# Kernel tuning notes

Hardware: AMD Instinct MI355X
Metric: run time of the kernel (lower is better)

## Reference

```python
import jax, jax.numpy as jnp
import numpy as np

N_ELEC = 62      # electrodes per graph (fixed by RGNN/SEED)
BATCH = 4096     # number of graphs
IN_CH = 5
HID = 32
N_CLS = 3
K = 2            # SGConv propagation steps (num_layers)


def setup_inputs() -> dict:
    key = jax.random.key(0)
    k1, k2, k3, k4 = jax.random.split(key, 4)
    n_tril = N_ELEC * (N_ELEC + 1) // 2  # 1953 learned lower-tri weights
    x = jax.random.normal(k1, (BATCH * N_ELEC, IN_CH), jnp.float32)
    adj_tril = jax.random.uniform(k2, (n_tril,), jnp.float32)
    lin_w = jax.random.normal(k3, (HID, IN_CH), jnp.float32) * 0.3
    lin_b = jnp.zeros((HID,), jnp.float32)
    fc_w = jax.random.normal(k4, (N_CLS, HID), jnp.float32) * 0.2
    fc_b = jnp.zeros((N_CLS,), jnp.float32)
    # Dense per-graph edge list matching adj.reshape(-1).repeat(B):
    # edge e = b*3844 + i*62 + j has source row=b*62+i, target col=b*62+j.
    i = np.arange(N_ELEC, dtype=np.int32)
    src = np.repeat(i, N_ELEC)              # [3844]
    dst = np.tile(i, N_ELEC)                # [3844]
    off = (np.arange(BATCH, dtype=np.int32) * N_ELEC)[:, None]
    row = (src[None, :] + off).reshape(-1)  # [B*3844]
    col = (dst[None, :] + off).reshape(-1)
    edge_index = jnp.asarray(np.stack([row, col]))  # int32 [2, E]
    batch_idx = jnp.asarray(np.repeat(np.arange(BATCH, dtype=np.int32), N_ELEC))
    return dict(x=x, adj_tril=adj_tril, lin_w=lin_w, lin_b=lin_b,
                fc_w=fc_w, fc_b=fc_b, edge_index=edge_index, batch_idx=batch_idx)


def reference(x, adj_tril, lin_w, lin_b, fc_w, fc_b, edge_index, batch_idx):
    # Rebuild symmetric dense adjacency from learned lower-triangular params.
    xs, ys = np.tril_indices(N_ELEC)  # static indices
    A = jnp.zeros((N_ELEC, N_ELEC), x.dtype).at[xs, ys].set(adj_tril)
    A = A + A.T - jnp.diag(jnp.diag(A))
    w = jnp.tile(A.reshape(-1), BATCH)        # edge weights [E]
    row, col = edge_index[0], edge_index[1]
    n_nodes = BATCH * N_ELEC
    # Symmetric GCN norm: D^-1/2 A D^-1/2 over the edge list (self-loops
    # already present in the dense graph, so add_remaining_self_loops is a
    # pure edge reorder here).
    deg = jax.ops.segment_sum(jnp.abs(w), row, num_segments=n_nodes)
    safe_deg = jnp.where(deg > 0, deg, 1.0)
    dinv = jnp.where(deg > 0, jax.lax.rsqrt(safe_deg), 0.0)
    norm = dinv[row] * w * dinv[col]          # [E]
    # K rounds of gather-scale-scatter propagation (SGConv).
    h = x
    for _ in range(K):
        h = jax.ops.segment_sum(norm[:, None] * h[row], col, num_segments=n_nodes)
    h = jax.nn.relu(h @ lin_w.T + lin_b)       # SGConv linear + relu
    pooled = jax.ops.segment_sum(h, batch_idx, num_segments=BATCH)  # global_add_pool
    # dropout is identity in eval mode
    return pooled @ fc_w.T + fc_b              # [B, num_classes]
```

## Files before the change

kernel.cpp:

```cpp
#include <hip/hip_runtime.h>

#define NE 62
#define IC 5
#define HID 32
#define NCLS 3
#define NGRAPH 4096
#define NTRIL 1953
#define SA 68
#define NM (NE*SA)

__global__ __launch_bounds__(256) void build_M(const float* __restrict__ adj_tril,
                                               float* __restrict__ Mg) {
    __shared__ float A[NE * SA];
    __shared__ float dinv[NE];
    int tid = threadIdx.x;
    for (int t = tid; t < NTRIL; t += 256) {
        float v = adj_tril[t];
        float r = sqrtf((float)(8 * t + 1));
        int i = (int)((r - 1.0f) * 0.5f);
        while ((i + 1) * (i + 2) / 2 <= t) ++i;
        while (i * (i + 1) / 2 > t) --i;
        int j = t - i * (i + 1) / 2;
        A[i * SA + j] = v;
        A[j * SA + i] = v;
    }
    __syncthreads();
    if (tid < NE) {
        float s = 0.f;
        for (int k = 0; k < NE; ++k) s += fabsf(A[tid * SA + k]);
        dinv[tid] = (s > 0.f) ? rsqrtf(s) : 0.f;
    }
    __syncthreads();
    for (int g = tid; g < NE * NE; g += 256) {
        int i = g / NE, j = g % NE;
        A[i * SA + j] *= dinv[i] * dinv[j];
    }
    __syncthreads();
    int g = blockIdx.x * 256 + tid;
    if (g < NE * NE) {
        int i = g / NE, j = g % NE;
        const float4* ra = (const float4*)(A + i * SA);
        const float4* rb = (const float4*)(A + j * SA);
        float acc = 0.f;
#pragma unroll
        for (int c = 0; c < 15; ++c) {
            float4 a = ra[c], b = rb[c];
            acc += a.x * b.x + a.y * b.y + a.z * b.z + a.w * b.w;
        }
        acc += A[i * SA + 60] * A[j * SA + 60] + A[i * SA + 61] * A[j * SA + 61];
        Mg[i * SA + j] = acc;
    }
}

__global__ __launch_bounds__(256) void forward_k(const float* __restrict__ x,
        const float* __restrict__ lin_w, const float* __restrict__ lin_b,
        const float* __restrict__ fc_w, const float* __restrict__ fc_b,
        const float* __restrict__ Mg, float* __restrict__ out) {
    __shared__ float Mlds[NM];
    __shared__ float Ys[4][NE * 12];
    int tid = threadIdx.x;
    {
        const float4* src = (const float4*)Mg;
        float4* dst = (float4*)Mlds;
        for (int t = tid; t < NM / 4; t += 256) dst[t] = src[t];
    }
    int wid = tid >> 6;
    int lane = tid & 63;
    int b = blockIdx.x * 4 + wid;
    int bu = __builtin_amdgcn_readfirstlane(b);
    const float* xg = x + (size_t)bu * (NE * IC);
    int c = lane & 31;
    float w0 = lin_w[c * 5 + 0], w1 = lin_w[c * 5 + 1], w2 = lin_w[c * 5 + 2],
          w3 = lin_w[c * 5 + 3], w4 = lin_w[c * 5 + 4];
    float lb = lin_b[c];
    float f0 = fc_w[c], f1 = fc_w[32 + c], f2 = fc_w[64 + c];
    __syncthreads();
    int j = lane;
    if (j < NE) {
        float y0 = 0, y1 = 0, y2 = 0, y3 = 0, y4 = 0;
        const float4* Mrow = (const float4*)(Mlds + j * SA);
        for (int ch = 0; ch < 15; ++ch) {
            float4 m = Mrow[ch];
            const float* xi = xg + ch * 20;
            y0 += m.x * xi[0];  y1 += m.x * xi[1];  y2 += m.x * xi[2];  y3 += m.x * xi[3];  y4 += m.x * xi[4];
            y0 += m.y * xi[5];  y1 += m.y * xi[6];  y2 += m.y * xi[7];  y3 += m.y * xi[8];  y4 += m.y * xi[9];
            y0 += m.z * xi[10]; y1 += m.z * xi[11]; y2 += m.z * xi[12]; y3 += m.z * xi[13]; y4 += m.z * xi[14];
            y0 += m.w * xi[15]; y1 += m.w * xi[16]; y2 += m.w * xi[17]; y3 += m.w * xi[18]; y4 += m.w * xi[19];
        }
        float m60 = Mlds[j * SA + 60], m61 = Mlds[j * SA + 61];
        y0 += m60 * xg[300] + m61 * xg[305];
        y1 += m60 * xg[301] + m61 * xg[306];
        y2 += m60 * xg[302] + m61 * xg[307];
        y3 += m60 * xg[303] + m61 * xg[308];
        y4 += m60 * xg[304] + m61 * xg[309];
        float* yr = &Ys[wid][j * 12];
        *(float4*)yr = make_float4(y0, y1, y2, y3);
        yr[4] = y4;
    }
    __syncthreads();
    int half = lane >> 5;
    float acc = 0.f;
    int jbeg = half * 31;
    for (int t = 0; t < 31; ++t) {
        const float* yr = &Ys[wid][(jbeg + t) * 12];
        float4 yv = *(const float4*)yr;
        float d = yv.x * w0 + yv.y * w1 + yv.z * w2 + yv.w * w3 + yr[4] * w4 + lb;
        acc += fmaxf(d, 0.f);
    }
    acc += __shfl_xor(acc, 32, 64);
    float p0 = acc * f0, p1 = acc * f1, p2 = acc * f2;
#pragma unroll
    for (int m = 16; m >= 1; m >>= 1) {
        p0 += __shfl_xor(p0, m, 64);
        p1 += __shfl_xor(p1, m, 64);
        p2 += __shfl_xor(p2, m, 64);
    }
    if (lane == 0) {
        out[b * 3 + 0] = p0 + fc_b[0];
        out[b * 3 + 1] = p1 + fc_b[1];
        out[b * 3 + 2] = p2 + fc_b[2];
    }
}

extern "C" void kernel_launch(void* const* d_in, const int* in_sizes, int n_in,
                              void* d_out, int out_size, void* d_ws, size_t ws_size,
                              hipStream_t stream) {
    const float* x        = (const float*)d_in[0];
    const float* adj_tril = (const float*)d_in[1];
    const float* lin_w    = (const float*)d_in[2];
    const float* lin_b    = (const float*)d_in[3];
    const float* fc_w     = (const float*)d_in[4];
    const float* fc_b     = (const float*)d_in[5];
    float* out = (float*)d_out;
    float* Mg  = (float*)d_ws;

    build_M<<<16, 256, 0, stream>>>(adj_tril, Mg);
    forward_k<<<1024, 256, 0, stream>>>(x, lin_w, lin_b, fc_w, fc_b, Mg, out);
}
```

Measured before the change: 185.1 us.

## Reorder M into column-chunk layout and stage x tiles in LDS

M is now written in a chunk-major layout (groups of 4 columns across all rows, plus a tail block), so lanes read consecutive float4s from LDS without conflicts. Each block cooperatively loads the x data for its 4 graphs into shared memory with coalesced float2 loads, and the inner loop reads x from LDS as float4. Before, each lane read x through uniform scalar global loads. The change adds LDS usage and an extra staging phase, which may affect occupancy.

```diff
diff --git a/kernel.cpp b/kernel.cpp
--- a/kernel.cpp
+++ b/kernel.cpp
@@ -2,12 +2,9 @@
 
 #define NE 62
 #define IC 5
-#define HID 32
-#define NCLS 3
-#define NGRAPH 4096
 #define NTRIL 1953
 #define SA 68
-#define NM (NE*SA)
+#define MTOT 3844
 
 __global__ __launch_bounds__(256) void build_M(const float* __restrict__ adj_tril,
                                                float* __restrict__ Mg) {
@@ -38,17 +35,19 @@
     __syncthreads();
     int g = blockIdx.x * 256 + tid;
     if (g < NE * NE) {
-        int i = g / NE, j = g % NE;
-        const float4* ra = (const float4*)(A + i * SA);
-        const float4* rb = (const float4*)(A + j * SA);
+        int r = g / NE, cidx = g % NE;
+        const float4* ra = (const float4*)(A + r * SA);
+        const float4* rb = (const float4*)(A + cidx * SA);
         float acc = 0.f;
 #pragma unroll
         for (int c = 0; c < 15; ++c) {
             float4 a = ra[c], b = rb[c];
             acc += a.x * b.x + a.y * b.y + a.z * b.z + a.w * b.w;
         }
-        acc += A[i * SA + 60] * A[j * SA + 60] + A[i * SA + 61] * A[j * SA + 61];
-        Mg[i * SA + j] = acc;
+        acc += A[r * SA + 60] * A[cidx * SA + 60] + A[r * SA + 61] * A[cidx * SA + 61];
+        int addr = (cidx < 60) ? ((cidx >> 2) * 248 + r * 4 + (cidx & 3))
+                               : (3720 + r * 2 + (cidx - 60));
+        Mg[addr] = acc;
     }
 }
 
@@ -56,19 +55,23 @@
         const float* __restrict__ lin_w, const float* __restrict__ lin_b,
         const float* __restrict__ fc_w, const float* __restrict__ fc_b,
         const float* __restrict__ Mg, float* __restrict__ out) {
-    __shared__ float Mlds[NM];
+    __shared__ float Mlds[MTOT];
+    __shared__ float Xs[4 * 312];
     __shared__ float Ys[4][NE * 12];
     int tid = threadIdx.x;
     {
         const float4* src = (const float4*)Mg;
         float4* dst = (float4*)Mlds;
-        for (int t = tid; t < NM / 4; t += 256) dst[t] = src[t];
+        for (int t = tid; t < MTOT / 4; t += 256) dst[t] = src[t];
+        const float2* xsrc = (const float2*)(x + (size_t)blockIdx.x * (4 * 310));
+        for (int t = tid; t < 620; t += 256) {
+            int w = t / 155, o = t - w * 155;
+            *(float2*)&Xs[w * 312 + o * 2] = xsrc[t];
+        }
     }
     int wid = tid >> 6;
     int lane = tid & 63;
     int b = blockIdx.x * 4 + wid;
-    int bu = __builtin_amdgcn_readfirstlane(b);
-    const float* xg = x + (size_t)bu * (NE * IC);
     int c = lane & 31;
     float w0 = lin_w[c * 5 + 0], w1 = lin_w[c * 5 + 1], w2 = lin_w[c * 5 + 2],
           w3 = lin_w[c * 5 + 3], w4 = lin_w[c * 5 + 4];
@@ -77,22 +80,25 @@
     __syncthreads();
     int j = lane;
     if (j < NE) {
+        const float* xb = Xs + wid * 312;
         float y0 = 0, y1 = 0, y2 = 0, y3 = 0, y4 = 0;
-        const float4* Mrow = (const float4*)(Mlds + j * SA);
+#pragma unroll
         for (int ch = 0; ch < 15; ++ch) {
-            float4 m = Mrow[ch];
-            const float* xi = xg + ch * 20;
-            y0 += m.x * xi[0];  y1 += m.x * xi[1];  y2 += m.x * xi[2];  y3 += m.x * xi[3];  y4 += m.x * xi[4];
-            y0 += m.y * xi[5];  y1 += m.y * xi[6];  y2 += m.y * xi[7];  y3 += m.y * xi[8];  y4 += m.y * xi[9];
-            y0 += m.z * xi[10]; y1 += m.z * xi[11]; y2 += m.z * xi[12]; y3 += m.z * xi[13]; y4 += m.z * xi[14];
-            y0 += m.w * xi[15]; y1 += m.w * xi[16]; y2 += m.w * xi[17]; y3 += m.w * xi[18]; y4 += m.w * xi[19];
+            float4 m = *(const float4*)(Mlds + ch * 248 + j * 4);
+            const float4* xi = (const float4*)(xb + ch * 20);
+            float4 xa = xi[0], xv = xi[1], xc = xi[2], xd = xi[3], xe = xi[4];
+            y0 += m.x * xa.x; y1 += m.x * xa.y; y2 += m.x * xa.z; y3 += m.x * xa.w; y4 += m.x * xv.x;
+            y0 += m.y * xv.y; y1 += m.y * xv.z; y2 += m.y * xv.w; y3 += m.y * xc.x; y4 += m.y * xc.y;
+            y0 += m.z * xc.z; y1 += m.z * xc.w; y2 += m.z * xd.x; y3 += m.z * xd.y; y4 += m.z * xd.z;
+            y0 += m.w * xd.w; y1 += m.w * xe.x; y2 += m.w * xe.y; y3 += m.w * xe.z; y4 += m.w * xe.w;
         }
-        float m60 = Mlds[j * SA + 60], m61 = Mlds[j * SA + 61];
-        y0 += m60 * xg[300] + m61 * xg[305];
-        y1 += m60 * xg[301] + m61 * xg[306];
-        y2 += m60 * xg[302] + m61 * xg[307];
-        y3 += m60 * xg[303] + m61 * xg[308];
-        y4 += m60 * xg[304] + m61 * xg[309];
+        float2 mt = *(const float2*)(Mlds + 3720 + j * 2);
+        const float* xt = xb + 300;
+        y0 += mt.x * xt[0] + mt.y * xt[5];
+        y1 += mt.x * xt[1] + mt.y * xt[6];
+        y2 += mt.x * xt[2] + mt.y * xt[7];
+        y3 += mt.x * xt[3] + mt.y * xt[8];
+        y4 += mt.x * xt[4] + mt.y * xt[9];
         float* yr = &Ys[wid][j * 12];
         *(float4*)yr = make_float4(y0, y1, y2, y3);
         yr[4] = y4;
```

Measured after the change: 184.3 us. No clear change (-0.4%).
